# Optimization experiments

Hardware: AMD Instinct MI355X
Metric: run time of the kernel (lower is better)

Reference implementation:

```python
import jax, jax.numpy as jnp
import numpy as np
import math

N_HEAD = 16
EPS = 1e-5
GELU_C = math.sqrt(2.0 / math.pi)

def _layernorm(v, w):
    # LN with weight only (bias=None), matching the module's quirky constructor
    mu = jnp.mean(v, axis=-1, keepdims=True)
    var = jnp.mean(jnp.square(v - mu), axis=-1, keepdims=True)
    return (v - mu) * jax.lax.rsqrt(var + EPS) * w

def _new_gelu(x):
    return 0.5 * x * (1.0 + jnp.tanh(GELU_C * (x + 0.044715 * x ** 3)))

def setup_inputs() -> dict:
    key = jax.random.key(0)
    k1, k2, k3, k4 = jax.random.split(key, 4)
    B, T, C = 2, 2048, 2048
    x = jax.random.normal(k1, (B, T, C), dtype=jnp.float32)
    w_qkv = jax.random.normal(k2, (C, 3 * C), dtype=jnp.float32) * 0.02
    w1 = jax.random.normal(k3, (C, 4 * C), dtype=jnp.float32) * 0.02
    w2 = jax.random.normal(k4, (4 * C, C), dtype=jnp.float32) * 0.02
    ln_w = jnp.ones((C,), dtype=jnp.float32)
    return {"x": x, "w_qkv": w_qkv, "w1": w1, "w2": w2, "ln_w": ln_w}

def reference(x, w_qkv, w1, w2, ln_w):
    B, T, C = x.shape
    H = N_HEAD
    D = C // H
    # --- attention branch (pre-LN, shared ln weight) ---
    h = _layernorm(x, ln_w)
    qkv = h @ w_qkv  # [B,T,3C]
    q, k, v = jnp.split(qkv, 3, axis=-1)
    q = q.reshape(B, T, H, D)
    k = k.reshape(B, T, H, D)
    v = v.reshape(B, T, H, D)
    scale = 1.0 / math.sqrt(D)
    att = jnp.einsum('bthd,bshd->bhts', q, k) * scale  # [B,H,T,T]
    causal = jnp.tril(jnp.ones((T, T), dtype=bool))
    att = jnp.where(causal, att, -jnp.inf)
    att = jax.nn.softmax(att, axis=-1)
    attn_out = jnp.einsum('bhts,bshd->bthd', att, v).reshape(B, T, C)
    x = x + attn_out  # note: no output projection in this module
    # --- MLP branch (same ln weight reused) ---
    h2 = _layernorm(x, ln_w)
    mlp = _new_gelu(h2 @ w1) @ w2
    return x + mlp
```

## Files before the change

### kernel.cpp

```cpp
#include <hip/hip_runtime.h>
#include <hip/hip_bf16.h>
#include <math.h>

typedef __bf16 BF16;
typedef __attribute__((ext_vector_type(8))) __bf16 bf16x8;
typedef __attribute__((ext_vector_type(4))) float f32x4;

__device__ __forceinline__ void gld_lds16(const void* g, void* l) {
    __builtin_amdgcn_global_load_lds(
        (__attribute__((address_space(1))) void*)(const void*)g,
        (__attribute__((address_space(3))) void*)l, 16, 0, 0);
}

template <int N> __device__ __forceinline__ void vmwait() {
    asm volatile("s_waitcnt vmcnt(%0)" :: "i"(N));
}

__global__ __launch_bounds__(256) void lnorm(const float* __restrict__ x,
                                             const float* __restrict__ w,
                                             BF16* __restrict__ out) {
    const int row = blockIdx.x, tid = threadIdx.x;
    const float* xr = x + (size_t)row * 2048;
    float4 a = *(const float4*)(xr + tid * 8);
    float4 b = *(const float4*)(xr + tid * 8 + 4);
    float s1 = a.x + a.y + a.z + a.w + b.x + b.y + b.z + b.w;
    float s2 = a.x*a.x + a.y*a.y + a.z*a.z + a.w*a.w +
               b.x*b.x + b.y*b.y + b.z*b.z + b.w*b.w;
    #pragma unroll
    for (int off = 32; off; off >>= 1) {
        s1 += __shfl_xor(s1, off);
        s2 += __shfl_xor(s2, off);
    }
    __shared__ float red[8];
    const int l = tid & 63, wv = tid >> 6;
    if (l == 0) { red[wv] = s1; red[4 + wv] = s2; }
    __syncthreads();
    s1 = red[0] + red[1] + red[2] + red[3];
    s2 = red[4] + red[5] + red[6] + red[7];
    const float mean = s1 * (1.0f / 2048.0f);
    const float var  = s2 * (1.0f / 2048.0f) - mean * mean;
    const float rstd = rsqrtf(var + 1e-5f);
    float4 wa = *(const float4*)(w + tid * 8);
    float4 wb = *(const float4*)(w + tid * 8 + 4);
    bf16x8 o;
    o[0] = (BF16)((a.x - mean) * rstd * wa.x);
    o[1] = (BF16)((a.y - mean) * rstd * wa.y);
    o[2] = (BF16)((a.z - mean) * rstd * wa.z);
    o[3] = (BF16)((a.w - mean) * rstd * wa.w);
    o[4] = (BF16)((b.x - mean) * rstd * wb.x);
    o[5] = (BF16)((b.y - mean) * rstd * wb.y);
    o[6] = (BF16)((b.z - mean) * rstd * wb.z);
    o[7] = (BF16)((b.w - mean) * rstd * wb.w);
    *(bf16x8*)(out + (size_t)row * 2048 + tid * 8) = o;
}

__global__ __launch_bounds__(256) void wtrans(const float* __restrict__ W,
                                              BF16* __restrict__ Wt,
                                              int K, int N) {
    __shared__ BF16 tile[32][33];
    const int n0 = blockIdx.x * 32, k0 = blockIdx.y * 32;
    const int tx = threadIdx.x, ty = threadIdx.y;
    #pragma unroll
    for (int i = 0; i < 4; i++)
        tile[ty + 8 * i][tx] = (BF16)W[(size_t)(k0 + ty + 8 * i) * N + n0 + tx];
    __syncthreads();
    #pragma unroll
    for (int i = 0; i < 4; i++)
        Wt[(size_t)(n0 + ty + 8 * i) * K + k0 + tx] = tile[tx][ty + 8 * i];
}

__global__ __launch_bounds__(256) void vtrans(const BF16* __restrict__ qkv,
                                              BF16* __restrict__ vT) {
    __shared__ BF16 tile[32][33];
    const int t0 = blockIdx.x * 32, d0 = blockIdx.y * 32, bh = blockIdx.z;
    const int b = bh >> 4, h = bh & 15;
    const int tx = threadIdx.x, ty = threadIdx.y;
    const BF16* src = qkv + (size_t)b * 2048 * 6144 + 4096 + h * 128;
    #pragma unroll
    for (int i = 0; i < 4; i++)
        tile[ty + 8 * i][tx] = src[(size_t)(t0 + ty + 8 * i) * 6144 + d0 + tx];
    __syncthreads();
    BF16* dst = vT + (size_t)bh * 128 * 2048;
    #pragma unroll
    for (int i = 0; i < 4; i++)
        dst[(size_t)(d0 + ty + 8 * i) * 2048 + t0 + tx] = tile[tx][ty + 8 * i];
}


#define STA(SI, TS) do { \
    _Pragma("unroll") \
    for (int j_ = 0; j_ < 2; ++j_) { \
        const int r_ = j_ * 128 + (tid >> 2); \
        const int sl_ = (tid & 3) ^ ((r_ >> 1) & 3); \
        gld_lds16(A + (size_t)(m0 + r_) * K + (TS) * 32 + sl_ * 8, \
                  Ab + (SI) * 16384 + j_ * 8192 + w * 1024); \
    } \
} while (0)

#define STB(SI, TS) do { \
    { \
        const int r_ = (tid >> 2); \
        const int sl_ = (tid & 3) ^ ((r_ >> 1) & 3); \
        gld_lds16(Bt + (size_t)(n0 + r_) * K + (TS) * 32 + sl_ * 8, \
                  Bb + (SI) * 8192 + w * 1024); \
    } \
} while (0)

#define LDA(BI, M_) \
    (*(const bf16x8*)(Ab + (BI) * 16384 + \
        (wm * 128 + (M_) * 16 + c) * 64 + ((g ^ fa) << 4)))

#define LDB(BI, N_) \
    (*(const bf16x8*)(Bb + (BI) * 8192 + \
        (wn * 32 + (N_) * 16 + c) * 64 + ((g ^ fa) << 4)))

#define GB3(BI, T, ST, VW) do { \
    vmwait<(VW)>(); \
    __builtin_amdgcn_s_barrier(); \
    __builtin_amdgcn_sched_barrier(0); \
    if (ST) { STB(((BI) + 2) % 3, (T) + 2); STA(((BI) + 2) % 3, (T) + 2); } \
    bf16x8 bfr[2], af[8]; \
    _Pragma("unroll") for (int n_ = 0; n_ < 2; ++n_) bfr[n_] = LDB(BI, n_); \
    _Pragma("unroll") for (int m_ = 0; m_ < 8; ++m_) af[m_] = LDA(BI, m_); \
    __builtin_amdgcn_s_setprio(1); \
    _Pragma("unroll") \
    for (int m_ = 0; m_ < 8; ++m_) \
      _Pragma("unroll") \
      for (int n_ = 0; n_ < 2; ++n_) \
        acc[m_][n_] = __builtin_amdgcn_mfma_f32_16x16x32_bf16( \
            af[m_], bfr[n_], acc[m_][n_], 0, 0, 0); \
    __builtin_amdgcn_s_setprio(0); \
} while (0)

template <int MODE>
__global__ __launch_bounds__(512, 4) void gemmP(const BF16* __restrict__ A,
                                                const BF16* __restrict__ Bt,
                                                void* __restrict__ out,
                                                const float* __restrict__ resid,
                                                int M, int N, int K) {
    (void)M;
    extern __shared__ char smem[];
    char* const Ab = smem;
    char* const Bb = smem + 49152;

    const int tid = threadIdx.x, l = tid & 63, w = tid >> 6;
    const int wm = w >> 2, wn = w & 3;
    const int g = l >> 4, c = l & 15;
    const int fa = (c >> 1) & 3;

    const int NBX = N >> 7;
    const int cpx = (int)gridDim.x >> 3;
    const int bid = (int)blockIdx.x;
    const int wg  = (bid & 7) * cpx + (bid >> 3);
    const int m0 = (wg / NBX) * 256, n0 = (wg % NBX) * 128;

    f32x4 acc[8][2] = {};

    STB(0, 0); STA(0, 0);
    STB(1, 1); STA(1, 1);

    const int NT = K >> 5;
    const int MAIN = NT - 4;
    for (int t = 0; t < MAIN; t += 3) {
        GB3(0, t,     1, 3);
        GB3(1, t + 1, 1, 3);
        GB3(2, t + 2, 1, 3);
    }
    GB3(0, MAIN,     1, 3);
    GB3(1, MAIN + 1, 1, 3);
    GB3(2, MAIN + 2, 0, 3);
    GB3(0, MAIN + 3, 0, 0);

    #pragma unroll
    for (int mi = 0; mi < 8; mi++)
      #pragma unroll
      for (int ni = 0; ni < 2; ni++)
        #pragma unroll
        for (int j = 0; j < 4; j++) {
            const int row = m0 + wm * 128 + mi * 16 + g * 4 + j;
            const int col = n0 + wn * 32 + ni * 16 + c;
            const float v = acc[mi][ni][j];
            const size_t idx = (size_t)row * N + col;
            if (MODE == 0) {
                ((BF16*)out)[idx] = (BF16)v;
            } else if (MODE == 1) {
                const float t2 = v + 0.044715f * v * v * v;
                const float s = 1.0f / (1.0f + __expf(-1.5957691216057308f * t2));
                ((BF16*)out)[idx] = (BF16)(v * s);
            } else {
                ((float*)out)[idx] = resid[idx] + v;
            }
        }
}

__global__ __launch_bounds__(256) void attn(const BF16* __restrict__ qkv,
                                            const BF16* __restrict__ vT,
                                            const float* __restrict__ x,
                                            float* __restrict__ x2) {
    __shared__ BF16 Ks[2][64 * 128];
    __shared__ BF16 Vs[2][128 * 64];
    __shared__ BF16 Ps[4][16 * 72];
    const int tid = threadIdx.x, l = tid & 63, w = tid >> 6;
    const int g = l >> 4, c = l & 15;
    const int bid = (int)blockIdx.x;
    const int wg = (bid & 7) * 64 + (bid >> 3);
    const int pair = wg & 15, bh = wg >> 4;
    const int b = bh >> 4, h = bh & 15;
    const int xr = (c & 7) << 4;

    const BF16* qbase = qkv + (size_t)b * 2048 * 6144 + h * 128;
    const char* kbase = (const char*)(qbase + 2048);
    const char* vbase = (const char*)(vT + (size_t)bh * 128 * 2048);

    auto STAGE = [&](int bb, int k0) {
        #pragma unroll
        for (int s = 0; s < 4; ++s) {
            const int rK = (w * 4 + s) * 4 + (l >> 4);
            const int cK = ((l & 15) * 16) ^ ((rK & 7) << 4);
            gld_lds16(kbase + (size_t)(k0 + rK) * 12288 + cK,
                      &Ks[bb][(w * 4 + s) * 512]);
            const int rV = (w * 4 + s) * 8 + (l >> 3);
            const int cV = ((l & 7) * 16) ^ ((rV & 7) << 4);
            gld_lds16(vbase + (size_t)rV * 4096 + (size_t)k0 * 2 + cV,
                      &Vs[bb][(w * 4 + s) * 512]);
        }
    };

    const float scale = 0.08838834764831845f;

    #pragma unroll 1
    for (int seg = 0; seg < 2; ++seg) {
        const int qb = seg ? 31 - pair : pair;
        const int q0 = qb * 64;

        bf16x8 qf[4];
        {
            const BF16* qrow = qbase + (size_t)(q0 + w * 16 + c) * 6144 + g * 8;
            #pragma unroll
            for (int kc = 0; kc < 4; kc++)
                qf[kc] = *(const bf16x8*)(qrow + kc * 32);
        }
        float m[4]    = {-1e30f, -1e30f, -1e30f, -1e30f};
        float lsum[4] = {0.f, 0.f, 0.f, 0.f};
        f32x4 O[8] = {};

        STAGE(0, 0);
        #pragma unroll 1
        for (int kt = 0; kt <= qb; ++kt) {
            if (kt < qb) { STAGE((kt + 1) & 1, (kt + 1) * 64); vmwait<8>(); }
            else vmwait<0>();
            __builtin_amdgcn_s_barrier();
            __builtin_amdgcn_sched_barrier(0);
            const char* KsB = (const char*)Ks[kt & 1];
            const char* VsB = (const char*)Vs[kt & 1];

            f32x4 s4[4] = {};
            #pragma unroll
            for (int ni = 0; ni < 4; ni++)
                #pragma unroll
                for (int kc = 0; kc < 4; kc++) {
                    const bf16x8 kf = *(const bf16x8*)(KsB +
                        (ni * 16 + c) * 256 + ((kc * 64 + g * 16) ^ xr));
                    s4[ni] = __builtin_amdgcn_mfma_f32_16x16x32_bf16(
                        qf[kc], kf, s4[ni], 0, 0, 0);
                }

            const bool maskt = (kt == qb);
            float sv[4][4];
            #pragma unroll
            for (int ni = 0; ni < 4; ni++)
                #pragma unroll
                for (int j = 0; j < 4; j++) {
                    const float v = s4[ni][j] * scale;
                    sv[ni][j] = (!maskt || (ni * 16 + c <= w * 16 + g * 4 + j))
                              ? v : -1e30f;
                }

            float sf[4];
            #pragma unroll
            for (int j = 0; j < 4; j++) {
                float tm = fmaxf(fmaxf(sv[0][j], sv[1][j]),
                                 fmaxf(sv[2][j], sv[3][j]));
                tm = fmaxf(tm, __shfl_xor(tm, 1));
                tm = fmaxf(tm, __shfl_xor(tm, 2));
                tm = fmaxf(tm, __shfl_xor(tm, 4));
                tm = fmaxf(tm, __shfl_xor(tm, 8));
                const float mn = fmaxf(m[j], tm);
                sf[j] = __expf(m[j] - mn);
                m[j] = mn;
            }

            float rs[4] = {0.f, 0.f, 0.f, 0.f};
            #pragma unroll
            for (int ni = 0; ni < 4; ni++)
                #pragma unroll
                for (int j = 0; j < 4; j++) {
                    const float p = __expf(sv[ni][j] - m[j]);
                    rs[j] += p;
                    Ps[w][(g * 4 + j) * 72 + ni * 16 + c] = (BF16)p;
                }
            #pragma unroll
            for (int j = 0; j < 4; j++) {
                float t = rs[j];
                t += __shfl_xor(t, 1);
                t += __shfl_xor(t, 2);
                t += __shfl_xor(t, 4);
                t += __shfl_xor(t, 8);
                lsum[j] = lsum[j] * sf[j] + t;
            }
            #pragma unroll
            for (int dn = 0; dn < 8; dn++)
                #pragma unroll
                for (int j = 0; j < 4; j++) O[dn][j] *= sf[j];

            bf16x8 pa[2];
            #pragma unroll
            for (int ks = 0; ks < 2; ks++)
                pa[ks] = *(const bf16x8*)((const char*)Ps[w] +
                             c * 144 + ks * 64 + g * 16);
            #pragma unroll
            for (int dn = 0; dn < 8; dn++)
                #pragma unroll
                for (int ks = 0; ks < 2; ks++) {
                    const bf16x8 vf = *(const bf16x8*)(VsB +
                        (dn * 16 + c) * 128 + ((ks * 64 + g * 16) ^ xr));
                    O[dn] = __builtin_amdgcn_mfma_f32_16x16x32_bf16(
                        pa[ks], vf, O[dn], 0, 0, 0);
                }
            __builtin_amdgcn_s_barrier();
            __builtin_amdgcn_sched_barrier(0);
        }

        float inv[4];
        #pragma unroll
        for (int j = 0; j < 4; j++) inv[j] = 1.0f / lsum[j];
        #pragma unroll
        for (int dn = 0; dn < 8; dn++)
            #pragma unroll
            for (int j = 0; j < 4; j++) {
                const int t   = q0 + w * 16 + g * 4 + j;
                const int col = h * 128 + dn * 16 + c;
                const size_t idx = ((size_t)b * 2048 + t) * 2048 + col;
                x2[idx] = x[idx] + O[dn][j] * inv[j];
            }
    }
}

extern "C" void kernel_launch(void* const* d_in, const int* in_sizes, int n_in,
                              void* d_out, int out_size, void* d_ws, size_t ws_size,
                              hipStream_t stream) {
    const float* x     = (const float*)d_in[0];
    const float* w_qkv = (const float*)d_in[1];
    const float* w1    = (const float*)d_in[2];
    const float* w2    = (const float*)d_in[3];
    const float* ln_w  = (const float*)d_in[4];
    float* out = (float*)d_out;

    char* ws = (char*)d_ws;
    BF16* h_buf = (BF16*)ws;  ws += (size_t)4096 * 2048 * 2;
    BF16* qkvb  = (BF16*)ws;  ws += (size_t)4096 * 6144 * 2;
    BF16* vTb   = (BF16*)ws;  ws += (size_t)32 * 128 * 2048 * 2;
    BF16* wqkvT = (BF16*)ws;  ws += (size_t)6144 * 2048 * 2;
    BF16* w1T   = (BF16*)ws;  ws += (size_t)8192 * 2048 * 2;
    BF16* w2T   = (BF16*)ws;  ws += (size_t)2048 * 8192 * 2;
    BF16* mlp1  = (BF16*)ws;  ws += (size_t)4096 * 8192 * 2;

    hipFuncSetAttribute((const void*)&gemmP<0>,
                        hipFuncAttributeMaxDynamicSharedMemorySize, 73728);
    hipFuncSetAttribute((const void*)&gemmP<1>,
                        hipFuncAttributeMaxDynamicSharedMemorySize, 73728);
    hipFuncSetAttribute((const void*)&gemmP<2>,
                        hipFuncAttributeMaxDynamicSharedMemorySize, 73728);

    lnorm<<<4096, 256, 0, stream>>>(x, ln_w, h_buf);
    wtrans<<<dim3(192, 64), dim3(32, 8), 0, stream>>>(w_qkv, wqkvT, 2048, 6144);
    gemmP<0><<<768, 512, 73728, stream>>>(
        h_buf, wqkvT, qkvb, nullptr, 4096, 6144, 2048);
    vtrans<<<dim3(64, 4, 32), dim3(32, 8), 0, stream>>>(qkvb, vTb);
    attn<<<512, 256, 0, stream>>>(qkvb, vTb, x, out);

    lnorm<<<4096, 256, 0, stream>>>(out, ln_w, h_buf);
    wtrans<<<dim3(256, 64), dim3(32, 8), 0, stream>>>(w1, w1T, 2048, 8192);
    gemmP<1><<<1024, 512, 73728, stream>>>(
        h_buf, w1T, mlp1, nullptr, 4096, 8192, 2048);
    wtrans<<<dim3(64, 256), dim3(32, 8), 0, stream>>>(w2, w2T, 8192, 2048);
    gemmP<2><<<256, 512, 73728, stream>>>(
        mlp1, w2T, out, out, 4096, 2048, 8192);
}
```

Before: 576.1 us.

## Use 256x256 tile, 4-stage pipelined GEMM for the QKV projection

Adds a new GEMM kernel, gemmN, with 256x256 output tiles per 512-thread block and a 4-deep LDS ring of 128KB. It issues the global-to-LDS prefetch after the fragment reads and places the wait and barrier at the end of each step. This kernel replaces the 256x128 three-stage gemmP for the QKV projection, with half as many blocks. The aim is higher arithmetic intensity per LDS byte and better latency hiding. The cost is lower occupancy (one block per CU because of the 128KB LDS), more accumulator registers, and fewer blocks (384) to spread over the CUs.

```diff
diff --git a/kernel.cpp b/kernel.cpp
--- a/kernel.cpp
+++ b/kernel.cpp
@@ -87,7 +87,7 @@
 }
 
 
-#define STA(SI, TS) do { \
+#define STA_N(SI, TS) do { \
     _Pragma("unroll") \
     for (int j_ = 0; j_ < 2; ++j_) { \
         const int r_ = j_ * 128 + (tid >> 2); \
@@ -97,7 +97,109 @@
     } \
 } while (0)
 
-#define STB(SI, TS) do { \
+#define STB_N(SI, TS) do { \
+    _Pragma("unroll") \
+    for (int j_ = 0; j_ < 2; ++j_) { \
+        const int r_ = j_ * 128 + (tid >> 2); \
+        const int sl_ = (tid & 3) ^ ((r_ >> 1) & 3); \
+        gld_lds16(Bt + (size_t)(n0 + r_) * K + (TS) * 32 + sl_ * 8, \
+                  Bb + (SI) * 16384 + j_ * 8192 + w * 1024); \
+    } \
+} while (0)
+
+#define LDA_N(BI, M_) \
+    (*(const bf16x8*)(Ab + (BI) * 16384 + \
+        (wm * 128 + (M_) * 16 + c) * 64 + ((g ^ fa) << 4)))
+
+#define LDB_N(BI, N_) \
+    (*(const bf16x8*)(Bb + (BI) * 16384 + \
+        (wn * 64 + (N_) * 16 + c) * 64 + ((g ^ fa) << 4)))
+
+#define GB_N(BI, T, DS, VW) do { \
+    bf16x8 bfr[4], af[8]; \
+    _Pragma("unroll") for (int n_ = 0; n_ < 4; ++n_) bfr[n_] = LDB_N(BI, n_); \
+    _Pragma("unroll") for (int m_ = 0; m_ < 8; ++m_) af[m_] = LDA_N(BI, m_); \
+    if (DS) { STB_N(((BI) + 3) & 3, (T) + 3); STA_N(((BI) + 3) & 3, (T) + 3); } \
+    _Pragma("unroll") \
+    for (int m_ = 0; m_ < 8; ++m_) \
+      _Pragma("unroll") \
+      for (int n_ = 0; n_ < 4; ++n_) \
+        acc[m_][n_] = __builtin_amdgcn_mfma_f32_16x16x32_bf16( \
+            af[m_], bfr[n_], acc[m_][n_], 0, 0, 0); \
+    vmwait<(VW)>(); \
+    __builtin_amdgcn_s_barrier(); \
+    __builtin_amdgcn_sched_barrier(0); \
+} while (0)
+
+template <int MODE>
+__global__ __launch_bounds__(512) void gemmN(const BF16* __restrict__ A,
+                                             const BF16* __restrict__ Bt,
+                                             void* __restrict__ out,
+                                             const float* __restrict__ resid,
+                                             int M, int N, int K) {
+    (void)M; (void)resid;
+    extern __shared__ char smem[];
+    char* const Ab = smem;
+    char* const Bb = smem + 65536;
+
+    const int tid = threadIdx.x, l = tid & 63, w = tid >> 6;
+    const int wm = w >> 2, wn = w & 3;
+    const int g = l >> 4, c = l & 15;
+    const int fa = (c >> 1) & 3;
+
+    const int NBX = N >> 8;
+    const int cpx = (int)gridDim.x >> 3;
+    const int bid = (int)blockIdx.x;
+    const int wg  = (bid & 7) * cpx + (bid >> 3);
+    const int m0 = (wg / NBX) * 256, n0 = (wg % NBX) * 256;
+
+    f32x4 acc[8][4] = {};
+
+    STB_N(0, 0); STA_N(0, 0);
+    STB_N(1, 1); STA_N(1, 1);
+    STB_N(2, 2); STA_N(2, 2);
+    vmwait<8>();
+    __builtin_amdgcn_s_barrier();
+    __builtin_amdgcn_sched_barrier(0);
+
+    const int NT = K >> 5;
+    for (int t = 0; t < NT - 4; t += 4) {
+        GB_N(0, t,     1, 8);
+        GB_N(1, t + 1, 1, 8);
+        GB_N(2, t + 2, 1, 8);
+        GB_N(3, t + 3, 1, 8);
+    }
+    GB_N(0, NT - 4, 1, 8);
+    GB_N(1, NT - 3, 0, 4);
+    GB_N(2, NT - 2, 0, 0);
+    GB_N(3, NT - 1, 0, 0);
+
+    #pragma unroll
+    for (int mi = 0; mi < 8; mi++)
+      #pragma unroll
+      for (int ni = 0; ni < 4; ni++)
+        #pragma unroll
+        for (int j = 0; j < 4; j++) {
+            const int row = m0 + wm * 128 + mi * 16 + g * 4 + j;
+            const int col = n0 + wn * 64 + ni * 16 + c;
+            const float v = acc[mi][ni][j];
+            const size_t idx = (size_t)row * N + col;
+            ((BF16*)out)[idx] = (BF16)v;
+        }
+}
+
+
+#define STA_P(SI, TS) do { \
+    _Pragma("unroll") \
+    for (int j_ = 0; j_ < 2; ++j_) { \
+        const int r_ = j_ * 128 + (tid >> 2); \
+        const int sl_ = (tid & 3) ^ ((r_ >> 1) & 3); \
+        gld_lds16(A + (size_t)(m0 + r_) * K + (TS) * 32 + sl_ * 8, \
+                  Ab + (SI) * 16384 + j_ * 8192 + w * 1024); \
+    } \
+} while (0)
+
+#define STB_P(SI, TS) do { \
     { \
         const int r_ = (tid >> 2); \
         const int sl_ = (tid & 3) ^ ((r_ >> 1) & 3); \
@@ -106,22 +208,22 @@
     } \
 } while (0)
 
-#define LDA(BI, M_) \
+#define LDA_P(BI, M_) \
     (*(const bf16x8*)(Ab + (BI) * 16384 + \
         (wm * 128 + (M_) * 16 + c) * 64 + ((g ^ fa) << 4)))
 
-#define LDB(BI, N_) \
+#define LDB_P(BI, N_) \
     (*(const bf16x8*)(Bb + (BI) * 8192 + \
         (wn * 32 + (N_) * 16 + c) * 64 + ((g ^ fa) << 4)))
 
-#define GB3(BI, T, ST, VW) do { \
+#define GB_P(BI, T, ST, VW) do { \
     vmwait<(VW)>(); \
     __builtin_amdgcn_s_barrier(); \
     __builtin_amdgcn_sched_barrier(0); \
-    if (ST) { STB(((BI) + 2) % 3, (T) + 2); STA(((BI) + 2) % 3, (T) + 2); } \
+    if (ST) { STB_P(((BI) + 2) % 3, (T) + 2); STA_P(((BI) + 2) % 3, (T) + 2); } \
     bf16x8 bfr[2], af[8]; \
-    _Pragma("unroll") for (int n_ = 0; n_ < 2; ++n_) bfr[n_] = LDB(BI, n_); \
-    _Pragma("unroll") for (int m_ = 0; m_ < 8; ++m_) af[m_] = LDA(BI, m_); \
+    _Pragma("unroll") for (int n_ = 0; n_ < 2; ++n_) bfr[n_] = LDB_P(BI, n_); \
+    _Pragma("unroll") for (int m_ = 0; m_ < 8; ++m_) af[m_] = LDA_P(BI, m_); \
     __builtin_amdgcn_s_setprio(1); \
     _Pragma("unroll") \
     for (int m_ = 0; m_ < 8; ++m_) \
@@ -156,20 +258,20 @@
 
     f32x4 acc[8][2] = {};
 
-    STB(0, 0); STA(0, 0);
-    STB(1, 1); STA(1, 1);
+    STB_P(0, 0); STA_P(0, 0);
+    STB_P(1, 1); STA_P(1, 1);
 
     const int NT = K >> 5;
     const int MAIN = NT - 4;
     for (int t = 0; t < MAIN; t += 3) {
-        GB3(0, t,     1, 3);
-        GB3(1, t + 1, 1, 3);
-        GB3(2, t + 2, 1, 3);
+        GB_P(0, t,     1, 3);
+        GB_P(1, t + 1, 1, 3);
+        GB_P(2, t + 2, 1, 3);
     }
-    GB3(0, MAIN,     1, 3);
-    GB3(1, MAIN + 1, 1, 3);
-    GB3(2, MAIN + 2, 0, 3);
-    GB3(0, MAIN + 3, 0, 0);
+    GB_P(0, MAIN,     1, 3);
+    GB_P(1, MAIN + 1, 1, 3);
+    GB_P(2, MAIN + 2, 0, 3);
+    GB_P(0, MAIN + 3, 0, 0);
 
     #pragma unroll
     for (int mi = 0; mi < 8; mi++)
@@ -181,9 +283,7 @@
             const int col = n0 + wn * 32 + ni * 16 + c;
             const float v = acc[mi][ni][j];
             const size_t idx = (size_t)row * N + col;
-            if (MODE == 0) {
-                ((BF16*)out)[idx] = (BF16)v;
-            } else if (MODE == 1) {
+            if (MODE == 1) {
                 const float t2 = v + 0.044715f * v * v * v;
                 const float s = 1.0f / (1.0f + __expf(-1.5957691216057308f * t2));
                 ((BF16*)out)[idx] = (BF16)(v * s);
@@ -365,8 +465,8 @@
     BF16* w2T   = (BF16*)ws;  ws += (size_t)2048 * 8192 * 2;
     BF16* mlp1  = (BF16*)ws;  ws += (size_t)4096 * 8192 * 2;
 
-    hipFuncSetAttribute((const void*)&gemmP<0>,
-                        hipFuncAttributeMaxDynamicSharedMemorySize, 73728);
+    hipFuncSetAttribute((const void*)&gemmN<0>,
+                        hipFuncAttributeMaxDynamicSharedMemorySize, 131072);
     hipFuncSetAttribute((const void*)&gemmP<1>,
                         hipFuncAttributeMaxDynamicSharedMemorySize, 73728);
     hipFuncSetAttribute((const void*)&gemmP<2>,
@@ -374,7 +474,7 @@
 
     lnorm<<<4096, 256, 0, stream>>>(x, ln_w, h_buf);
     wtrans<<<dim3(192, 64), dim3(32, 8), 0, stream>>>(w_qkv, wqkvT, 2048, 6144);
-    gemmP<0><<<768, 512, 73728, stream>>>(
+    gemmN<0><<<384, 512, 131072, stream>>>(
         h_buf, wqkvT, qkvb, nullptr, 4096, 6144, 2048);
     vtrans<<<dim3(64, 4, 32), dim3(32, 8), 0, stream>>>(qkvb, vTb);
     attn<<<512, 256, 0, stream>>>(qkvb, vTb, x, out);
```

After: 571.6 us. About the same (-0.8%).
